# Kernel optimization log

Hardware: AMD Instinct MI355X
Metric: run time of the kernel (lower is better)

Reference implementation:

```python
import jax, jax.numpy as jnp
import numpy as np

B, N, E, D = 4, 2048, 2048, 2048  # batch, seq, embedding_dim, out_dim


def setup_inputs() -> dict:
    key = jax.random.key(0)
    k1, k2, k3 = jax.random.split(key, 3)
    x = jax.random.normal(k1, (B, N, E), dtype=jnp.float32)
    # qkv_proj: Linear(E, 3*D). Store weight as [E, 3D] for x @ W.
    W = jax.random.normal(k2, (E, 3 * D), dtype=jnp.float32) * (1.0 / np.sqrt(E))
    b = jax.random.normal(k3, (3 * D,), dtype=jnp.float32) * 0.01
    return {"x": x, "W": W, "b": b}


def reference(x, W, b):
    d = W.shape[1] // 3
    n = x.shape[1]
    qkv = x @ W + b                                   # [B, N, 3D]
    q, k, v = jnp.split(qkv, 3, axis=-1)              # each [B, N, D]
    scale = 1.0 / np.sqrt(d).astype(np.float32)
    att = jnp.einsum('bqd,bkd->bqk', q, k) * scale    # [B, N, N]
    causal = jnp.tril(jnp.ones((n, n), dtype=bool))
    att = jnp.where(causal[None, :, :], att, -jnp.inf)
    # softmax_with_denom: stable softmax, also return the denominator
    m = jnp.max(att, axis=-1, keepdims=True)
    e = jnp.exp(att - m)
    denom = jnp.sum(e, axis=-1)                       # [B, N]
    p = e / denom[..., None]
    y = jnp.einsum('bqk,bkd->bqd', p, v)              # [B, N, D]
    return y, denom
```

## Files before the change

### kernel.cpp

```cpp
#include <hip/hip_runtime.h>

typedef unsigned short u16;
typedef unsigned int   u32;

#define SEQ 2048
#define EMB 2048
#define TD  6144

using bf16x8 = __attribute__((ext_vector_type(8))) __bf16;
using f32x4  = __attribute__((ext_vector_type(4))) float;
using u16x8v = __attribute__((ext_vector_type(8))) u16;

typedef __attribute__((address_space(1))) const void* gas_t;
typedef __attribute__((address_space(3))) void*       las_t;
#define GLOAD16(g, l) __builtin_amdgcn_global_load_lds((gas_t)(g), (las_t)(l), 16, 0, 0)

__device__ __forceinline__ u16 f2bf(float f) {
  u32 u = __float_as_uint(f);
  u += 0x7fffu + ((u >> 16) & 1u);
  return (u16)(u >> 16);
}

__global__ __launch_bounds__(256) void cast_x_kern(const float* __restrict__ x,
                                                   u16* __restrict__ xb) {
  size_t i = ((size_t)blockIdx.x * 256 + threadIdx.x) * 4;
  float4 v = *(const float4*)(x + i);
  ushort4 u;
  u.x = f2bf(v.x); u.y = f2bf(v.y); u.z = f2bf(v.z); u.w = f2bf(v.w);
  *(ushort4*)(xb + i) = u;
}

__global__ __launch_bounds__(256) void castT_W_kern(const float* __restrict__ W,
                                                    u16* __restrict__ Wt) {
  __shared__ float t[64][65];
  int c0 = blockIdx.x * 64, r0 = blockIdx.y * 64;
  int tid = threadIdx.x;
#pragma unroll
  for (int i = 0; i < 4; ++i) {
    int flat = i * 1024 + tid * 4;
    int r = flat >> 6, c = flat & 63;
    float4 v = *(const float4*)(W + (size_t)(r0 + r) * TD + c0 + c);
    t[r][c] = v.x; t[r][c + 1] = v.y; t[r][c + 2] = v.z; t[r][c + 3] = v.w;
  }
  __syncthreads();
#pragma unroll
  for (int i = 0; i < 4; ++i) {
    int flat = i * 1024 + tid * 4;
    int wr = flat >> 6, wc = flat & 63;
    ushort4 u;
    u.x = f2bf(t[wc + 0][wr]); u.y = f2bf(t[wc + 1][wr]);
    u.z = f2bf(t[wc + 2][wr]); u.w = f2bf(t[wc + 3][wr]);
    *(ushort4*)(Wt + (size_t)(c0 + wr) * EMB + r0 + wc) = u;
  }
}

template <int MODE>
__global__ __launch_bounds__(512, 2) void gemm256(const u16* __restrict__ Ab,
                                                  const u16* __restrict__ Bb,
                                                  void* __restrict__ Cb,
                                                  void* __restrict__ Cb2,
                                                  const float* __restrict__ bias) {
  __shared__ char lds[2][65536];

  constexpr int lda = (MODE == 0) ? EMB : 4096;
  constexpr int ldb = (MODE == 0) ? EMB : (MODE == 1) ? 4096 : SEQ;
  constexpr int NWG = (MODE == 0) ? 768 : (MODE == 1) ? 144 : 256;
  constexpr int CPX = NWG / 8;

  int bid = blockIdx.x;
  int wg = (bid & 7) * CPX + (bid >> 3);

  const u16 *A, *Bt;
  int row0, col0, nk;
  size_t coff = 0;
  if constexpr (MODE == 0) {
    A = Ab; Bt = Bb;
    row0 = (wg / 24) * 256; col0 = (wg % 24) * 256; nk = EMB / 64;
  } else if constexpr (MODE == 1) {
    int b = wg / 36, tq = wg % 36;
    int qi = (int)((sqrtf(8.f * (float)tq + 1.f) - 1.f) * 0.5f);
    while ((qi + 1) * (qi + 2) / 2 <= tq) ++qi;
    while (qi * (qi + 1) / 2 > tq) --qi;
    int kj = tq - qi * (qi + 1) / 2;
    A = Ab + (size_t)b * SEQ * 4096;
    Bt = A + 2048;
    row0 = qi * 256; col0 = kj * 256; nk = EMB / 64;
    coff = (size_t)b * SEQ * SEQ;
  } else {
    int b = wg >> 6, qi = (wg >> 3) & 7, nj = wg & 7;
    A = Ab + (size_t)b * SEQ * 4096;
    Bt = Bb + (size_t)b * SEQ * SEQ;
    row0 = qi * 256; col0 = nj * 256; nk = (qi + 1) * 4;
    coff = (size_t)b * SEQ * SEQ;
  }

  int tid = threadIdx.x;
  int wave = tid >> 6, lane = tid & 63;
  int wm = wave >> 2, wn = wave & 3;

  int sbase[8];
#pragma unroll
  for (int i = 0; i < 4; ++i) sbase[i] = 32768 + i * 8192 + wave * 1024;
#pragma unroll
  for (int i = 0; i < 4; ++i)
    sbase[4 + i] = i * 4096 + ((wave < 4) ? wave * 1024 : 16384 + (wave - 4) * 1024);

  auto stageb = [&](int bi, int t, int buf) {
    int ob = sbase[bi];
    int obl = ob + lane * 16;
    int row = (obl & 32767) >> 7;
    int cb = obl & 127;
    int c = ((cb ^ ((row & 7) << 4)) >> 1) + t * 64;
    const u16* src = (ob < 32768) ? (A + (size_t)(row0 + row) * lda + c)
                                  : (Bt + (size_t)(col0 + row) * ldb + c);
    GLOAD16(src, (char*)&lds[buf][0] + ob);
  };

  auto ldA = [&](int buf, int rr, int ks) -> bf16x8 {
    int cb = ks * 64 + (lane >> 4) * 16;
    return *(const bf16x8*)&lds[buf][rr * 128 + (cb ^ ((rr & 7) << 4))];
  };
  auto ldB = [&](int buf, int rr, int ks) -> bf16x8 {
    int cb = ks * 64 + (lane >> 4) * 16;
    return *(const bf16x8*)&lds[buf][32768 + rr * 128 + (cb ^ ((rr & 7) << 4))];
  };

  f32x4 acc[8][4];
#pragma unroll
  for (int m = 0; m < 8; ++m)
#pragma unroll
    for (int n = 0; n < 4; ++n) acc[m][n] = (f32x4){0.f, 0.f, 0.f, 0.f};

#pragma unroll
  for (int bi = 0; bi < 8; ++bi) stageb(bi, 0, 0);
#pragma unroll
  for (int bi = 0; bi < 6; ++bi) stageb(bi, 1, 1);
  asm volatile("s_waitcnt vmcnt(6)" ::: "memory");
  __builtin_amdgcn_s_barrier();

  bf16x8 bfg[4][2];
  for (int t = 0; t < nk; ++t) {
    int cur = t & 1, nxt = cur ^ 1;
    bool pf1 = (t + 1 < nk), pf2 = (t + 2 < nk);
    bf16x8 afg[2][2];

#pragma unroll
    for (int n = 0; n < 4; ++n)
#pragma unroll
      for (int ks = 0; ks < 2; ++ks)
        bfg[n][ks] = ldB(cur, wn * 64 + n * 16 + (lane & 15), ks);
#pragma unroll
    for (int m = 0; m < 2; ++m)
#pragma unroll
      for (int ks = 0; ks < 2; ++ks)
        afg[m][ks] = ldA(cur, wm * 128 + m * 16 + (lane & 15), ks);
    if (pf1) { stageb(6, t + 1, nxt); stageb(7, t + 1, nxt); }
    __builtin_amdgcn_s_setprio(1);
#pragma unroll
    for (int m = 0; m < 2; ++m)
#pragma unroll
      for (int n = 0; n < 4; ++n)
#pragma unroll
        for (int ks = 0; ks < 2; ++ks)
          acc[m][n] = __builtin_amdgcn_mfma_f32_16x16x32_bf16(
              afg[m][ks], bfg[n][ks], acc[m][n], 0, 0, 0);
    __builtin_amdgcn_s_setprio(0);
    __builtin_amdgcn_s_barrier();

#pragma unroll
    for (int m = 0; m < 2; ++m)
#pragma unroll
      for (int ks = 0; ks < 2; ++ks)
        afg[m][ks] = ldA(cur, wm * 128 + (2 + m) * 16 + (lane & 15), ks);
    if (pf2) { stageb(0, t + 2, cur); stageb(1, t + 2, cur); }
    __builtin_amdgcn_s_setprio(1);
#pragma unroll
    for (int m = 0; m < 2; ++m)
#pragma unroll
      for (int n = 0; n < 4; ++n)
#pragma unroll
        for (int ks = 0; ks < 2; ++ks)
          acc[2 + m][n] = __builtin_amdgcn_mfma_f32_16x16x32_bf16(
              afg[m][ks], bfg[n][ks], acc[2 + m][n], 0, 0, 0);
    __builtin_amdgcn_s_setprio(0);

#pragma unroll
    for (int m = 0; m < 2; ++m)
#pragma unroll
      for (int ks = 0; ks < 2; ++ks)
        afg[m][ks] = ldA(cur, wm * 128 + (4 + m) * 16 + (lane & 15), ks);
    if (pf2) { stageb(2, t + 2, cur); stageb(3, t + 2, cur); }
    __builtin_amdgcn_s_setprio(1);
#pragma unroll
    for (int m = 0; m < 2; ++m)
#pragma unroll
      for (int n = 0; n < 4; ++n)
#pragma unroll
        for (int ks = 0; ks < 2; ++ks)
          acc[4 + m][n] = __builtin_amdgcn_mfma_f32_16x16x32_bf16(
              afg[m][ks], bfg[n][ks], acc[4 + m][n], 0, 0, 0);
    __builtin_amdgcn_s_setprio(0);
    __builtin_amdgcn_s_barrier();

#pragma unroll
    for (int m = 0; m < 2; ++m)
#pragma unroll
      for (int ks = 0; ks < 2; ++ks)
        afg[m][ks] = ldA(cur, wm * 128 + (6 + m) * 16 + (lane & 15), ks);
    if (pf2) { stageb(4, t + 2, cur); stageb(5, t + 2, cur); }
    __builtin_amdgcn_s_setprio(1);
#pragma unroll
    for (int m = 0; m < 2; ++m)
#pragma unroll
      for (int n = 0; n < 4; ++n)
#pragma unroll
        for (int ks = 0; ks < 2; ++ks)
          acc[6 + m][n] = __builtin_amdgcn_mfma_f32_16x16x32_bf16(
              afg[m][ks], bfg[n][ks], acc[6 + m][n], 0, 0, 0);
    __builtin_amdgcn_s_setprio(0);
    if (pf2)      asm volatile("s_waitcnt vmcnt(6)" ::: "memory");
    else if (pf1) asm volatile("s_waitcnt vmcnt(0)" ::: "memory");
    __builtin_amdgcn_s_barrier();
  }

  int ln = lane & 15;
  int l4 = (lane >> 4) << 2;
  int rb = row0 + wm * 128, cb0 = col0 + wn * 64;
  if constexpr (MODE == 0) {
    if (col0 < 4096) {
      u16* C = (u16*)Cb;
#pragma unroll
      for (int n = 0; n < 4; ++n) {
        float bv = bias[cb0 + n * 16 + ln];
#pragma unroll
        for (int m = 0; m < 8; ++m)
#pragma unroll
          for (int r = 0; r < 4; ++r)
            C[(size_t)(rb + m * 16 + l4 + r) * 4096 + cb0 + n * 16 + ln] =
                f2bf(acc[m][n][r] + bv);
      }
    } else {
      u16* vTb = (u16*)Cb2 + (size_t)(row0 >> 11) * SEQ * SEQ;
      int nbase = row0 & 2047;
      u16 (*T)[264] = (u16(*)[264])(&lds[0][0]);
      int half = wn >> 1;
      int dloc0 = (wn & 1) * 64;
#pragma unroll
      for (int hh = 0; hh < 2; ++hh) {
        if (half == hh) {
#pragma unroll
          for (int n = 0; n < 4; ++n) {
            float bv = bias[cb0 + n * 16 + ln];
            int dl = dloc0 + n * 16 + ln;
#pragma unroll
            for (int m = 0; m < 8; ++m) {
              int nn = wm * 128 + m * 16 + l4;
#pragma unroll
              for (int r = 0; r < 4; ++r)
                T[dl][nn + r] = f2bf(acc[m][n][r] + bv);
            }
          }
        }
        __syncthreads();
        int dl = tid >> 5, nn = (tid & 31) * 8;
#pragma unroll
        for (int it = 0; it < 8; ++it) {
          int loc = it * 16 + dl;
          *(u16x8v*)&vTb[(size_t)(col0 - 4096 + hh * 128 + loc) * SEQ + nbase + nn] =
              *(const u16x8v*)&T[loc][nn];
        }
        __syncthreads();
      }
    }
  } else if constexpr (MODE == 1) {
    float* C = (float*)Cb + coff;
    const float scale = 0.022097086912079608f;
#pragma unroll
    for (int m = 0; m < 8; ++m)
#pragma unroll
      for (int n = 0; n < 4; ++n)
#pragma unroll
        for (int r = 0; r < 4; ++r)
          C[(size_t)(rb + m * 16 + l4 + r) * SEQ + cb0 + n * 16 + ln] =
              acc[m][n][r] * scale;
  } else {
    float* C = (float*)Cb + coff;
#pragma unroll
    for (int m = 0; m < 8; ++m)
#pragma unroll
      for (int n = 0; n < 4; ++n)
#pragma unroll
        for (int r = 0; r < 4; ++r)
          C[(size_t)(rb + m * 16 + l4 + r) * SEQ + cb0 + n * 16 + ln] = acc[m][n][r];
  }
}

__global__ __launch_bounds__(256) void softmax_kern(const float* __restrict__ att,
                                                    u16* __restrict__ P,
                                                    float* __restrict__ denom) {
  int row = blockIdx.x;
  int q = row & (SEQ - 1);
  const float* arow = att + (size_t)row * SEQ;
  u16* prow = P + (size_t)row * 4096;
  int jlen = ((q >> 8) + 1) << 8;
  int tid = threadIdx.x;
  int j0 = tid * 4, j1 = tid * 4 + 1024;
  float NI = -__builtin_inff();
  float4 a0 = make_float4(NI, NI, NI, NI), a1 = a0;
  if (j0 < jlen) a0 = *(const float4*)(arow + j0);
  if (j1 < jlen) a1 = *(const float4*)(arow + j1);
  if (j0 + 0 > q) a0.x = NI;
  if (j0 + 1 > q) a0.y = NI;
  if (j0 + 2 > q) a0.z = NI;
  if (j0 + 3 > q) a0.w = NI;
  if (j1 + 0 > q) a1.x = NI;
  if (j1 + 1 > q) a1.y = NI;
  if (j1 + 2 > q) a1.z = NI;
  if (j1 + 3 > q) a1.w = NI;
  float mx = fmaxf(fmaxf(fmaxf(a0.x, a0.y), fmaxf(a0.z, a0.w)),
                   fmaxf(fmaxf(a1.x, a1.y), fmaxf(a1.z, a1.w)));
#pragma unroll
  for (int off = 32; off; off >>= 1) mx = fmaxf(mx, __shfl_xor(mx, off, 64));
  __shared__ float red[8];
  int wv = tid >> 6;
  if ((tid & 63) == 0) red[wv] = mx;
  __syncthreads();
  mx = fmaxf(fmaxf(red[0], red[1]), fmaxf(red[2], red[3]));
  a0.x = expf(a0.x - mx); a0.y = expf(a0.y - mx);
  a0.z = expf(a0.z - mx); a0.w = expf(a0.w - mx);
  a1.x = expf(a1.x - mx); a1.y = expf(a1.y - mx);
  a1.z = expf(a1.z - mx); a1.w = expf(a1.w - mx);
  float s = (a0.x + a0.y + a0.z + a0.w) + (a1.x + a1.y + a1.z + a1.w);
#pragma unroll
  for (int off = 32; off; off >>= 1) s += __shfl_xor(s, off, 64);
  if ((tid & 63) == 0) red[4 + wv] = s;
  __syncthreads();
  s = red[4] + red[5] + red[6] + red[7];
  float inv = 1.0f / s;
  if (j0 < jlen) {
    ushort4 u;
    u.x = f2bf(a0.x * inv); u.y = f2bf(a0.y * inv);
    u.z = f2bf(a0.z * inv); u.w = f2bf(a0.w * inv);
    *(ushort4*)(prow + j0) = u;
  }
  if (j1 < jlen) {
    ushort4 u;
    u.x = f2bf(a1.x * inv); u.y = f2bf(a1.y * inv);
    u.z = f2bf(a1.z * inv); u.w = f2bf(a1.w * inv);
    *(ushort4*)(prow + j1) = u;
  }
  if (tid == 0) denom[row] = s;
}

extern "C" void kernel_launch(void* const* d_in, const int* in_sizes, int n_in,
                              void* d_out, int out_size, void* d_ws, size_t ws_size,
                              hipStream_t stream) {
  const float* x    = (const float*)d_in[0];
  const float* W    = (const float*)d_in[1];
  const float* bias = (const float*)d_in[2];

  if (ws_size < 201326592u) return;

  char* w = (char*)d_ws;
  u16*   qk  = (u16*)w;
  u16*   vT  = (u16*)(w + 67108864);
  u16*   xb  = (u16*)(w + 100663296);
  u16*   Wt  = (u16*)(w + 134217728);
  float* att = (float*)(w + 134217728);
  u16*   P   = (u16*)(w + 134217728);

  float* y     = (float*)d_out;
  float* denom = y + (size_t)4 * SEQ * SEQ;

  cast_x_kern<<<16384, 256, 0, stream>>>(x, xb);
  castT_W_kern<<<dim3(96, 32), 256, 0, stream>>>(W, Wt);
  gemm256<0><<<768, 512, 0, stream>>>(xb, Wt, qk, vT, bias);
  gemm256<1><<<144, 512, 0, stream>>>(qk, nullptr, att, nullptr, nullptr);
  softmax_kern<<<8192, 256, 0, stream>>>(att, P, denom);
  gemm256<2><<<256, 512, 0, stream>>>(P, vT, y, nullptr, nullptr);
}
```

Baseline: 334.4 us.

## Use 128x128 tiles for causal QK and PV GEMMs with finer triangle skipping

Splits the QKV projection into its own 256x256 kernel and adds a new 128x128-tile GEMM kernel (256 threads) for the QK^T and P·V stages. The smaller tiles follow the causal triangle more closely, so fewer masked blocks are computed. They also launch more workgroups (544 and 1024 instead of 144 and 256) for better CU occupancy. The PV grid issues the longest row blocks first to balance load. Softmax now zero-fills at 128-column granularity to match. The cost is lower per-tile data reuse and more global traffic per FLOP.

```diff
diff --git a/kernel.cpp b/kernel.cpp
--- a/kernel.cpp
+++ b/kernel.cpp
@@ -54,45 +54,18 @@
   }
 }
 
-template <int MODE>
-__global__ __launch_bounds__(512, 2) void gemm256(const u16* __restrict__ Ab,
-                                                  const u16* __restrict__ Bb,
-                                                  void* __restrict__ Cb,
-                                                  void* __restrict__ Cb2,
-                                                  const float* __restrict__ bias) {
+__global__ __launch_bounds__(512, 2) void gemm_qkv(const u16* __restrict__ Ab,
+                                                   const u16* __restrict__ Bb,
+                                                   u16* __restrict__ Cb,
+                                                   u16* __restrict__ Cb2,
+                                                   const float* __restrict__ bias) {
   __shared__ char lds[2][65536];
-
-  constexpr int lda = (MODE == 0) ? EMB : 4096;
-  constexpr int ldb = (MODE == 0) ? EMB : (MODE == 1) ? 4096 : SEQ;
-  constexpr int NWG = (MODE == 0) ? 768 : (MODE == 1) ? 144 : 256;
-  constexpr int CPX = NWG / 8;
-
+  constexpr int lda = EMB, ldb = EMB;
   int bid = blockIdx.x;
-  int wg = (bid & 7) * CPX + (bid >> 3);
-
-  const u16 *A, *Bt;
-  int row0, col0, nk;
-  size_t coff = 0;
-  if constexpr (MODE == 0) {
-    A = Ab; Bt = Bb;
-    row0 = (wg / 24) * 256; col0 = (wg % 24) * 256; nk = EMB / 64;
-  } else if constexpr (MODE == 1) {
-    int b = wg / 36, tq = wg % 36;
-    int qi = (int)((sqrtf(8.f * (float)tq + 1.f) - 1.f) * 0.5f);
-    while ((qi + 1) * (qi + 2) / 2 <= tq) ++qi;
-    while (qi * (qi + 1) / 2 > tq) --qi;
-    int kj = tq - qi * (qi + 1) / 2;
-    A = Ab + (size_t)b * SEQ * 4096;
-    Bt = A + 2048;
-    row0 = qi * 256; col0 = kj * 256; nk = EMB / 64;
-    coff = (size_t)b * SEQ * SEQ;
-  } else {
-    int b = wg >> 6, qi = (wg >> 3) & 7, nj = wg & 7;
-    A = Ab + (size_t)b * SEQ * 4096;
-    Bt = Bb + (size_t)b * SEQ * SEQ;
-    row0 = qi * 256; col0 = nj * 256; nk = (qi + 1) * 4;
-    coff = (size_t)b * SEQ * SEQ;
-  }
+  int wg = (bid & 7) * 96 + (bid >> 3);
+  const u16* A = Ab;
+  const u16* Bt = Bb;
+  int row0 = (wg / 24) * 256, col0 = (wg % 24) * 256, nk = EMB / 64;
 
   int tid = threadIdx.x;
   int wave = tid >> 6, lane = tid & 63;
@@ -115,7 +88,6 @@
                                   : (Bt + (size_t)(col0 + row) * ldb + c);
     GLOAD16(src, (char*)&lds[buf][0] + ob);
   };
-
   auto ldA = [&](int buf, int rr, int ks) -> bf16x8 {
     int cb = ks * 64 + (lane >> 4) * 16;
     return *(const bf16x8*)&lds[buf][rr * 128 + (cb ^ ((rr & 7) << 4))];
@@ -143,7 +115,6 @@
     int cur = t & 1, nxt = cur ^ 1;
     bool pf1 = (t + 1 < nk), pf2 = (t + 2 < nk);
     bf16x8 afg[2][2];
-
 #pragma unroll
     for (int n = 0; n < 4; ++n)
 #pragma unroll
@@ -166,7 +137,6 @@
               afg[m][ks], bfg[n][ks], acc[m][n], 0, 0, 0);
     __builtin_amdgcn_s_setprio(0);
     __builtin_amdgcn_s_barrier();
-
 #pragma unroll
     for (int m = 0; m < 2; ++m)
 #pragma unroll
@@ -183,7 +153,6 @@
           acc[2 + m][n] = __builtin_amdgcn_mfma_f32_16x16x32_bf16(
               afg[m][ks], bfg[n][ks], acc[2 + m][n], 0, 0, 0);
     __builtin_amdgcn_s_setprio(0);
-
 #pragma unroll
     for (int m = 0; m < 2; ++m)
 #pragma unroll
@@ -201,7 +170,6 @@
               afg[m][ks], bfg[n][ks], acc[4 + m][n], 0, 0, 0);
     __builtin_amdgcn_s_setprio(0);
     __builtin_amdgcn_s_barrier();
-
 #pragma unroll
     for (int m = 0; m < 2; ++m)
 #pragma unroll
@@ -226,73 +194,194 @@
   int ln = lane & 15;
   int l4 = (lane >> 4) << 2;
   int rb = row0 + wm * 128, cb0 = col0 + wn * 64;
-  if constexpr (MODE == 0) {
-    if (col0 < 4096) {
-      u16* C = (u16*)Cb;
-#pragma unroll
-      for (int n = 0; n < 4; ++n) {
-        float bv = bias[cb0 + n * 16 + ln];
-#pragma unroll
-        for (int m = 0; m < 8; ++m)
-#pragma unroll
-          for (int r = 0; r < 4; ++r)
-            C[(size_t)(rb + m * 16 + l4 + r) * 4096 + cb0 + n * 16 + ln] =
-                f2bf(acc[m][n][r] + bv);
-      }
-    } else {
-      u16* vTb = (u16*)Cb2 + (size_t)(row0 >> 11) * SEQ * SEQ;
-      int nbase = row0 & 2047;
-      u16 (*T)[264] = (u16(*)[264])(&lds[0][0]);
-      int half = wn >> 1;
-      int dloc0 = (wn & 1) * 64;
-#pragma unroll
-      for (int hh = 0; hh < 2; ++hh) {
-        if (half == hh) {
-#pragma unroll
-          for (int n = 0; n < 4; ++n) {
-            float bv = bias[cb0 + n * 16 + ln];
-            int dl = dloc0 + n * 16 + ln;
-#pragma unroll
-            for (int m = 0; m < 8; ++m) {
-              int nn = wm * 128 + m * 16 + l4;
-#pragma unroll
-              for (int r = 0; r < 4; ++r)
-                T[dl][nn + r] = f2bf(acc[m][n][r] + bv);
-            }
+  if (col0 < 4096) {
+    u16* C = Cb;
+#pragma unroll
+    for (int n = 0; n < 4; ++n) {
+      float bv = bias[cb0 + n * 16 + ln];
+#pragma unroll
+      for (int m = 0; m < 8; ++m)
+#pragma unroll
+        for (int r = 0; r < 4; ++r)
+          C[(size_t)(rb + m * 16 + l4 + r) * 4096 + cb0 + n * 16 + ln] =
+              f2bf(acc[m][n][r] + bv);
+    }
+  } else {
+    u16* vTb = Cb2 + (size_t)(row0 >> 11) * SEQ * SEQ;
+    int nbase = row0 & 2047;
+    u16 (*T)[264] = (u16(*)[264])(&lds[0][0]);
+    int half = wn >> 1;
+    int dloc0 = (wn & 1) * 64;
+#pragma unroll
+    for (int hh = 0; hh < 2; ++hh) {
+      if (half == hh) {
+#pragma unroll
+        for (int n = 0; n < 4; ++n) {
+          float bv = bias[cb0 + n * 16 + ln];
+          int dl = dloc0 + n * 16 + ln;
+#pragma unroll
+          for (int m = 0; m < 8; ++m) {
+            int nn = wm * 128 + m * 16 + l4;
+#pragma unroll
+            for (int r = 0; r < 4; ++r)
+              T[dl][nn + r] = f2bf(acc[m][n][r] + bv);
           }
         }
-        __syncthreads();
-        int dl = tid >> 5, nn = (tid & 31) * 8;
-#pragma unroll
-        for (int it = 0; it < 8; ++it) {
-          int loc = it * 16 + dl;
-          *(u16x8v*)&vTb[(size_t)(col0 - 4096 + hh * 128 + loc) * SEQ + nbase + nn] =
-              *(const u16x8v*)&T[loc][nn];
-        }
-        __syncthreads();
       }
+      __syncthreads();
+      int dl = tid >> 5, nn = (tid & 31) * 8;
+#pragma unroll
+      for (int it = 0; it < 8; ++it) {
+        int loc = it * 16 + dl;
+        *(u16x8v*)&vTb[(size_t)(col0 - 4096 + hh * 128 + loc) * SEQ + nbase + nn] =
+            *(const u16x8v*)&T[loc][nn];
+      }
+      __syncthreads();
     }
-  } else if constexpr (MODE == 1) {
-    float* C = (float*)Cb + coff;
-    const float scale = 0.022097086912079608f;
-#pragma unroll
-    for (int m = 0; m < 8; ++m)
-#pragma unroll
-      for (int n = 0; n < 4; ++n)
-#pragma unroll
-        for (int r = 0; r < 4; ++r)
-          C[(size_t)(rb + m * 16 + l4 + r) * SEQ + cb0 + n * 16 + ln] =
-              acc[m][n][r] * scale;
+  }
+}
+
+template <int MODE>
+__global__ __launch_bounds__(256, 2) void gemm128(const u16* __restrict__ Ab,
+                                                  const u16* __restrict__ Bb,
+                                                  float* __restrict__ Cb) {
+  __shared__ char lds[2][32768];
+  constexpr int lda = 4096;
+  constexpr int ldb = (MODE == 1) ? 4096 : SEQ;
+
+  int bid = blockIdx.x;
+  const u16 *A, *Bt;
+  int row0, col0, nk;
+  size_t coff;
+  if constexpr (MODE == 1) {
+    constexpr int CPX = 544 / 8;
+    int wg = (bid & 7) * CPX + (bid >> 3);
+    int b = wg / 136, tq = wg % 136;
+    int qi = (int)((sqrtf(8.f * (float)tq + 1.f) - 1.f) * 0.5f);
+    while ((qi + 1) * (qi + 2) / 2 <= tq) ++qi;
+    while (qi * (qi + 1) / 2 > tq) --qi;
+    int kj = tq - qi * (qi + 1) / 2;
+    A = Ab + (size_t)b * SEQ * 4096;
+    Bt = A + 2048;
+    row0 = qi * 128; col0 = kj * 128; nk = EMB / 64;
+    coff = (size_t)b * SEQ * SEQ;
   } else {
-    float* C = (float*)Cb + coff;
-#pragma unroll
-    for (int m = 0; m < 8; ++m)
-#pragma unroll
-      for (int n = 0; n < 4; ++n)
-#pragma unroll
-        for (int r = 0; r < 4; ++r)
-          C[(size_t)(rb + m * 16 + l4 + r) * SEQ + cb0 + n * 16 + ln] = acc[m][n][r];
-  }
+    int xcd = bid & 7, idx = bid >> 3;
+    int qi = 15 - (idx >> 3);
+    int g = xcd * 8 + (idx & 7);
+    int b = g >> 4, nj = g & 15;
+    A = Ab + (size_t)b * SEQ * 4096;
+    Bt = Bb + (size_t)b * SEQ * SEQ;
+    row0 = qi * 128; col0 = nj * 128; nk = (qi + 1) * 2;
+    coff = (size_t)b * SEQ * SEQ;
+  }
+
+  int tid = threadIdx.x;
+  int wave = tid >> 6, lane = tid & 63;
+  int wm = wave >> 1, wn = wave & 1;
+  int ln = lane & 15;
+
+  int sbase[8];
+#pragma unroll
+  for (int i = 0; i < 4; ++i) sbase[i] = 16384 + i * 4096 + wave * 1024;
+#pragma unroll
+  for (int i = 0; i < 4; ++i) sbase[4 + i] = i * 4096 + wave * 1024;
+
+  auto stageb = [&](int bi, int t, int buf) {
+    int ob = sbase[bi];
+    int obl = ob + lane * 16;
+    int row = (obl & 16383) >> 7;
+    int cb = obl & 127;
+    int c = ((cb ^ ((row & 7) << 4)) >> 1) + t * 64;
+    const u16* src = (ob < 16384) ? (A + (size_t)(row0 + row) * lda + c)
+                                  : (Bt + (size_t)(col0 + row) * ldb + c);
+    GLOAD16(src, (char*)&lds[buf][0] + ob);
+  };
+  auto ldA = [&](int buf, int rr, int ks) -> bf16x8 {
+    int cb = ks * 64 + (lane >> 4) * 16;
+    return *(const bf16x8*)&lds[buf][rr * 128 + (cb ^ ((rr & 7) << 4))];
+  };
+  auto ldB = [&](int buf, int rr, int ks) -> bf16x8 {
+    int cb = ks * 64 + (lane >> 4) * 16;
+    return *(const bf16x8*)&lds[buf][16384 + rr * 128 + (cb ^ ((rr & 7) << 4))];
+  };
+
+  f32x4 acc[4][4];
+#pragma unroll
+  for (int m = 0; m < 4; ++m)
+#pragma unroll
+    for (int n = 0; n < 4; ++n) acc[m][n] = (f32x4){0.f, 0.f, 0.f, 0.f};
+
+#pragma unroll
+  for (int bi = 0; bi < 8; ++bi) stageb(bi, 0, 0);
+  stageb(0, 1, 1); stageb(1, 1, 1); stageb(2, 1, 1); stageb(3, 1, 1);
+  stageb(4, 1, 1); stageb(6, 1, 1);
+  asm volatile("s_waitcnt vmcnt(6)" ::: "memory");
+  __builtin_amdgcn_s_barrier();
+
+  bf16x8 bfg[4][2];
+  for (int t = 0; t < nk; ++t) {
+    int cur = t & 1, nxt = cur ^ 1;
+    bool pf1 = (t + 1 < nk), pf2 = (t + 2 < nk);
+    bf16x8 afg[2][2];
+#pragma unroll
+    for (int n = 0; n < 4; ++n)
+#pragma unroll
+      for (int ks = 0; ks < 2; ++ks)
+        bfg[n][ks] = ldB(cur, wn * 64 + n * 16 + ln, ks);
+#pragma unroll
+    for (int m = 0; m < 2; ++m)
+#pragma unroll
+      for (int ks = 0; ks < 2; ++ks)
+        afg[m][ks] = ldA(cur, wm * 64 + m * 16 + ln, ks);
+    if (pf1) { stageb(5, t + 1, nxt); stageb(7, t + 1, nxt); }
+    __builtin_amdgcn_s_setprio(1);
+#pragma unroll
+    for (int m = 0; m < 2; ++m)
+#pragma unroll
+      for (int n = 0; n < 4; ++n)
+#pragma unroll
+        for (int ks = 0; ks < 2; ++ks)
+          acc[m][n] = __builtin_amdgcn_mfma_f32_16x16x32_bf16(
+              afg[m][ks], bfg[n][ks], acc[m][n], 0, 0, 0);
+    __builtin_amdgcn_s_setprio(0);
+    __builtin_amdgcn_s_barrier();
+#pragma unroll
+    for (int m = 0; m < 2; ++m)
+#pragma unroll
+      for (int ks = 0; ks < 2; ++ks)
+        afg[m][ks] = ldA(cur, wm * 64 + (2 + m) * 16 + ln, ks);
+    if (pf2) {
+      stageb(0, t + 2, cur); stageb(1, t + 2, cur); stageb(2, t + 2, cur);
+      stageb(3, t + 2, cur); stageb(4, t + 2, cur); stageb(6, t + 2, cur);
+    }
+    __builtin_amdgcn_s_setprio(1);
+#pragma unroll
+    for (int m = 0; m < 2; ++m)
+#pragma unroll
+      for (int n = 0; n < 4; ++n)
+#pragma unroll
+        for (int ks = 0; ks < 2; ++ks)
+          acc[2 + m][n] = __builtin_amdgcn_mfma_f32_16x16x32_bf16(
+              afg[m][ks], bfg[n][ks], acc[2 + m][n], 0, 0, 0);
+    __builtin_amdgcn_s_setprio(0);
+    if (pf2)      asm volatile("s_waitcnt vmcnt(6)" ::: "memory");
+    else if (pf1) asm volatile("s_waitcnt vmcnt(0)" ::: "memory");
+    __builtin_amdgcn_s_barrier();
+  }
+
+  int l4 = (lane >> 4) << 2;
+  int rb = row0 + wm * 64, cb0 = col0 + wn * 64;
+  float* C = Cb + coff;
+  const float scale = (MODE == 1) ? 0.022097086912079608f : 1.0f;
+#pragma unroll
+  for (int m = 0; m < 4; ++m)
+#pragma unroll
+    for (int n = 0; n < 4; ++n)
+#pragma unroll
+      for (int r = 0; r < 4; ++r)
+        C[(size_t)(rb + m * 16 + l4 + r) * SEQ + cb0 + n * 16 + ln] =
+            acc[m][n][r] * scale;
 }
 
 __global__ __launch_bounds__(256) void softmax_kern(const float* __restrict__ att,
@@ -302,7 +391,7 @@
   int q = row & (SEQ - 1);
   const float* arow = att + (size_t)row * SEQ;
   u16* prow = P + (size_t)row * 4096;
-  int jlen = ((q >> 8) + 1) << 8;
+  int jlen = ((q >> 7) + 1) << 7;
   int tid = threadIdx.x;
   int j0 = tid * 4, j1 = tid * 4 + 1024;
   float NI = -__builtin_inff();
@@ -374,8 +463,8 @@
 
   cast_x_kern<<<16384, 256, 0, stream>>>(x, xb);
   castT_W_kern<<<dim3(96, 32), 256, 0, stream>>>(W, Wt);
-  gemm256<0><<<768, 512, 0, stream>>>(xb, Wt, qk, vT, bias);
-  gemm256<1><<<144, 512, 0, stream>>>(qk, nullptr, att, nullptr, nullptr);
+  gemm_qkv<<<768, 512, 0, stream>>>(xb, Wt, qk, vT, bias);
+  gemm128<1><<<544, 256, 0, stream>>>(qk, nullptr, att);
   softmax_kern<<<8192, 256, 0, stream>>>(att, P, denom);
-  gemm256<2><<<256, 512, 0, stream>>>(P, vT, y, nullptr, nullptr);
-}
+  gemm128<2><<<1024, 256, 0, stream>>>(P, vT, y);
+}
```

Measured after the change: 328.9 us. No clear change (-1.6%).
